# Optimization experiments

Measured on AMD Instinct MI355X. Metric: run time of the kernel, lower is better.

Reference implementation:

```python
import jax, jax.numpy as jnp
import numpy as np

NB1, NB2, B1 = 4, 4, 48
IN_F, OUT_F = 4096, 4096
BATCH = 16384


def setup_inputs() -> dict:
    key = jax.random.key(0)
    k1, k2, k3, k4 = jax.random.split(key, 4)
    i = IN_F // NB1          # 1024, per-block input width
    l = OUT_F // NB2         # 1024, per-block output width
    x = jax.random.normal(k1, (BATCH, IN_F), jnp.float32)
    # kaiming-uniform-ish scale for the factors
    w1_bfly = jax.random.normal(k2, (NB1, NB2 * B1, i), jnp.float32) * (1.0 / np.sqrt(i))
    w2_bfly = jax.random.normal(k3, (NB2, l, NB1 * B1), jnp.float32) * (1.0 / np.sqrt(NB1 * B1))
    bias = jax.random.normal(k4, (OUT_F,), jnp.float32) * 0.01
    return {"x": x, "w1_bfly": w1_bfly, "w2_bfly": w2_bfly, "bias": bias}


def reference(x, w1_bfly, w2_bfly, bias):
    # blockdiag_butterfly_multiply_einsum (Monarch-style, two block-diagonal GEMMs)
    k, q, p = w1_bfly.shape   # k = nblocks1, q = nblocks2*b1, p = in/nblocks1
    l, s, r = w2_bfly.shape   # l = nblocks2, s = out/nblocks2, r = nblocks1*b1
    b1 = q // l
    batch = x.shape[0]
    xr = x.reshape(batch, k, p)
    # stage 1: block-diagonal matmul over nblocks1
    out1 = jnp.einsum('bkp,kqp->bkq', xr, w1_bfly)               # (b, k, l*b1)
    # block transpose: (b, k, (l b1)) -> (b, l, (k b1))
    out1 = out1.reshape(batch, k, l, b1).transpose(0, 2, 1, 3).reshape(batch, l, k * b1)
    # stage 2: block-diagonal matmul over nblocks2
    out2 = jnp.einsum('blr,lsr->bls', out1, w2_bfly)             # (b, l, s)
    return out2.reshape(batch, l * s) + bias
```

## Files before the change

kernel.cpp:

```cpp
#include <hip/hip_runtime.h>
#include <cstdint>
#include <cstddef>

typedef __attribute__((ext_vector_type(8))) short short8;
typedef __attribute__((ext_vector_type(4))) float f32x4;
typedef __attribute__((ext_vector_type(4))) short short4v;

__device__ __forceinline__ unsigned short f2bf(float f) {
  unsigned u = __builtin_bit_cast(unsigned, f);
  u += 0x7fffu + ((u >> 16) & 1u);
  return (unsigned short)(u >> 16);
}

__device__ __forceinline__ void gload_lds16(const unsigned short* g, unsigned short* l) {
  __builtin_amdgcn_global_load_lds(
      (__attribute__((address_space(1))) unsigned int*)g,
      (__attribute__((address_space(3))) unsigned int*)l, 16, 0, 0);
}

__global__ __launch_bounds__(256) void cvt_k(const float* __restrict__ src,
                                             unsigned short* __restrict__ dst, int n) {
  int i = (blockIdx.x * 256 + threadIdx.x) * 4;
  if (i + 3 < n) {
    float4 v = *(const float4*)(src + i);
    short4v o;
    o.x = (short)f2bf(v.x); o.y = (short)f2bf(v.y);
    o.z = (short)f2bf(v.z); o.w = (short)f2bf(v.w);
    *(short4v*)(dst + i) = o;
  }
}

__global__ __launch_bounds__(256, 4) void stage1_k(
    const float* __restrict__ x, const unsigned short* __restrict__ w1bf,
    unsigned short* __restrict__ Y) {
  __shared__ __attribute__((aligned(16))) unsigned short sh[(64 + 192) * 64];
  unsigned short* As = sh;
  unsigned short* Bs = sh + 64 * 64;
  const int t  = threadIdx.x;
  const int r0 = blockIdx.x * 64;
  const int kb = blockIdx.y;

  const int lane = t & 63;
  const int w  = t >> 6;
  const int wm = w & 1, wn = w >> 1;
  const int lm = lane & 15;
  const int lk = lane >> 4;

  f32x4 acc[2][6];
#pragma unroll
  for (int i = 0; i < 2; ++i)
#pragma unroll
    for (int j = 0; j < 6; ++j) acc[i][j] = (f32x4)0.0f;

  const float* xbase = x + (size_t)r0 * 4096 + kb * 1024;
  const unsigned short* wb = w1bf + (size_t)kb * 192 * 1024;
  const int ldsbase = (t & ~63) << 3;

  for (int kt = 0; kt < 16; ++kt) {
    const int k0 = kt * 64;
#pragma unroll
    for (int i = 0; i < 6; ++i) {
      int c = i * 256 + t;
      int row = c >> 3, slot = c & 7;
      gload_lds16(wb + (size_t)row * 1024 + k0 + ((slot ^ (row & 7)) << 3),
                  Bs + (i * 256 << 3) + ldsbase);
    }
#pragma unroll
    for (int j = 0; j < 2; ++j) {
      int u = t + 256 * j;
      int row = u >> 3, c8 = u & 7;
      const float* p = xbase + (size_t)row * 4096 + k0 + c8 * 8;
      float4 a0 = *(const float4*)p;
      float4 a1 = *(const float4*)(p + 4);
      short8 o;
      o[0] = (short)f2bf(a0.x); o[1] = (short)f2bf(a0.y);
      o[2] = (short)f2bf(a0.z); o[3] = (short)f2bf(a0.w);
      o[4] = (short)f2bf(a1.x); o[5] = (short)f2bf(a1.y);
      o[6] = (short)f2bf(a1.z); o[7] = (short)f2bf(a1.w);
      *(short8*)&As[(row << 6) + ((c8 ^ (row & 7)) << 3)] = o;
    }
    __syncthreads();
#pragma unroll
    for (int ks = 0; ks < 2; ++ks) {
      const int sl = ks * 4 + lk;
      short8 a[2], b[6];
#pragma unroll
      for (int rt = 0; rt < 2; ++rt) {
        int r = wm * 32 + rt * 16 + lm;
        a[rt] = *(const short8*)&As[(r << 6) + ((sl ^ (r & 7)) << 3)];
      }
#pragma unroll
      for (int ct = 0; ct < 6; ++ct) {
        int r = wn * 96 + ct * 16 + lm;
        b[ct] = *(const short8*)&Bs[(r << 6) + ((sl ^ (r & 7)) << 3)];
      }
#pragma unroll
      for (int rt = 0; rt < 2; ++rt)
#pragma unroll
        for (int ct = 0; ct < 6; ++ct)
          acc[rt][ct] = __builtin_amdgcn_mfma_f32_16x16x32_bf16(a[rt], b[ct], acc[rt][ct], 0, 0, 0);
    }
    __syncthreads();
  }

#pragma unroll
  for (int rt = 0; rt < 2; ++rt) {
#pragma unroll
    for (int ct = 0; ct < 6; ++ct) {
      int q  = wn * 96 + ct * 16 + lm;
      int li = q / 48, j = q - li * 48;
      size_t base = (size_t)(r0 + wm * 32 + rt * 16 + lk * 4) * 768 + li * 192 + kb * 48 + j;
#pragma unroll
      for (int reg = 0; reg < 4; ++reg)
        Y[base + (size_t)reg * 768] = f2bf(acc[rt][ct][reg]);
    }
  }
}

__global__ __launch_bounds__(256, 4) void stage2_k(
    const unsigned short* __restrict__ Y, const unsigned short* __restrict__ w2bf,
    const float* __restrict__ bias, float* __restrict__ out) {
  __shared__ __attribute__((aligned(16))) unsigned short sh[2 * 128 * 64];
  unsigned short* As = sh;
  unsigned short* Bs = sh + 128 * 64;

  int lin  = blockIdx.x;
  int virt = ((lin & 7) << 9) + (lin >> 3);
  const int n0 = (virt & 7) * 128;
  const int r0 = ((virt >> 3) & 127) * 128;
  const int l  = virt >> 10;

  const int t = threadIdx.x;
  const int lane = t & 63;
  const int w  = t >> 6;
  const int wm = w & 1, wn = w >> 1;
  const int lm = lane & 15;
  const int lk = lane >> 4;

  f32x4 acc[4][4];
#pragma unroll
  for (int i = 0; i < 4; ++i)
#pragma unroll
    for (int j = 0; j < 4; ++j) acc[i][j] = (f32x4)0.0f;

  const unsigned short* ybase = Y + (size_t)r0 * 768 + l * 192;
  const unsigned short* wbase = w2bf + (size_t)(l * 1024 + n0) * 192;
  const int ldsbase = (t & ~63) << 3;

  for (int kt = 0; kt < 3; ++kt) {
    const int k0 = kt * 64;
#pragma unroll
    for (int i = 0; i < 4; ++i) {
      int c = i * 256 + t;
      int row = c >> 3, slot = c & 7;
      int sc = k0 + ((slot ^ (row & 7)) << 3);
      gload_lds16(ybase + (size_t)row * 768 + sc, As + (i * 256 << 3) + ldsbase);
      gload_lds16(wbase + (size_t)row * 192 + sc, Bs + (i * 256 << 3) + ldsbase);
    }
    __syncthreads();
#pragma unroll
    for (int ks = 0; ks < 2; ++ks) {
      const int sl = ks * 4 + lk;
      short8 a[4], b[4];
#pragma unroll
      for (int rt = 0; rt < 4; ++rt) {
        int r = wm * 64 + rt * 16 + lm;
        a[rt] = *(const short8*)&As[(r << 6) + ((sl ^ (r & 7)) << 3)];
      }
#pragma unroll
      for (int ct = 0; ct < 4; ++ct) {
        int r = wn * 64 + ct * 16 + lm;
        b[ct] = *(const short8*)&Bs[(r << 6) + ((sl ^ (r & 7)) << 3)];
      }
#pragma unroll
      for (int rt = 0; rt < 4; ++rt)
#pragma unroll
        for (int ct = 0; ct < 4; ++ct)
          acc[rt][ct] = __builtin_amdgcn_mfma_f32_16x16x32_bf16(a[rt], b[ct], acc[rt][ct], 0, 0, 0);
    }
    __syncthreads();
  }

  float* LF = (float*)sh + w * 1088;
  float bv[4];
#pragma unroll
  for (int ct = 0; ct < 4; ++ct)
    bv[ct] = bias[l * 1024 + n0 + wn * 64 + ct * 16 + lm];

#pragma unroll
  for (int rt = 0; rt < 4; ++rt) {
#pragma unroll
    for (int ct = 0; ct < 4; ++ct)
#pragma unroll
      for (int reg = 0; reg < 4; ++reg)
        LF[(lk * 4 + reg) * 68 + ct * 16 + lm] = acc[rt][ct][reg] + bv[ct];
#pragma unroll
    for (int it = 0; it < 4; ++it) {
      int idx = it * 64 + lane;
      int rr = idx >> 4, cc = idx & 15;
      float4 vv = *(const float4*)&LF[rr * 68 + cc * 4];
      *(float4*)&out[(size_t)(r0 + wm * 64 + rt * 16 + rr) * 4096 + l * 1024 + n0 + wn * 64 + cc * 4] = vv;
    }
  }
}

extern "C" void kernel_launch(void* const* d_in, const int* in_sizes, int n_in,
                              void* d_out, int out_size, void* d_ws, size_t ws_size,
                              hipStream_t stream) {
  const float* x    = (const float*)d_in[0];
  const float* w1   = (const float*)d_in[1];
  const float* w2   = (const float*)d_in[2];
  const float* bias = (const float*)d_in[3];
  float* out = (float*)d_out;

  unsigned short* Y    = (unsigned short*)d_ws;
  unsigned short* w1bf = (unsigned short*)((char*)d_ws + 25165824);
  unsigned short* w2bf = (unsigned short*)((char*)d_ws + 25165824 + 1572864);

  cvt_k<<<768, 256, 0, stream>>>(w1, w1bf, 786432);
  cvt_k<<<768, 256, 0, stream>>>(w2, w2bf, 786432);
  stage1_k<<<dim3(256, 4), 256, 0, stream>>>(x, w1bf, Y);
  stage2_k<<<4096, 256, 0, stream>>>(Y, w2bf, bias, out);
}
```

Measured before the change: 508.7 us.

## Fuse both butterfly GEMM stages into one kernel keeping intermediate in LDS

Merges the stage-1 and stage-2 kernels into a single kernel where each block handles 32 rows, computes all four stage-1 blocks into a swizzled LDS tile, then runs stage 2 from that LDS tile with B fragments read straight from global memory. This removes the global round-trip of the bf16 intermediate and one launch, and the two weight-conversion launches are merged into one. It also adds register prefetch of the next x tile. In exchange the grid is only 512 blocks with 2 per CU, the M tile is small, which lowers weight reuse, and output stores are scalar and uncoalesced.

```diff
diff --git a/kernel.cpp b/kernel.cpp
--- a/kernel.cpp
+++ b/kernel.cpp
@@ -18,189 +18,151 @@
       (__attribute__((address_space(3))) unsigned int*)l, 16, 0, 0);
 }
 
-__global__ __launch_bounds__(256) void cvt_k(const float* __restrict__ src,
-                                             unsigned short* __restrict__ dst, int n) {
+__global__ __launch_bounds__(256) void cvt_k(const float* __restrict__ w1,
+                                             const float* __restrict__ w2,
+                                             unsigned short* __restrict__ w1bf,
+                                             unsigned short* __restrict__ w2bf) {
+  const float* src = blockIdx.y ? w2 : w1;
+  unsigned short* dst = blockIdx.y ? w2bf : w1bf;
   int i = (blockIdx.x * 256 + threadIdx.x) * 4;
-  if (i + 3 < n) {
-    float4 v = *(const float4*)(src + i);
-    short4v o;
-    o.x = (short)f2bf(v.x); o.y = (short)f2bf(v.y);
-    o.z = (short)f2bf(v.z); o.w = (short)f2bf(v.w);
-    *(short4v*)(dst + i) = o;
-  }
+  float4 v = *(const float4*)(src + i);
+  short4v o;
+  o.x = (short)f2bf(v.x); o.y = (short)f2bf(v.y);
+  o.z = (short)f2bf(v.z); o.w = (short)f2bf(v.w);
+  *(short4v*)(dst + i) = o;
 }
 
-__global__ __launch_bounds__(256, 4) void stage1_k(
+#define YT_SH (32 * 768)
+__global__ __launch_bounds__(256, 2) void fused_k(
     const float* __restrict__ x, const unsigned short* __restrict__ w1bf,
-    unsigned short* __restrict__ Y) {
-  __shared__ __attribute__((aligned(16))) unsigned short sh[(64 + 192) * 64];
-  unsigned short* As = sh;
-  unsigned short* Bs = sh + 64 * 64;
-  const int t  = threadIdx.x;
-  const int r0 = blockIdx.x * 64;
-  const int kb = blockIdx.y;
+    const unsigned short* __restrict__ w2bf, const float* __restrict__ bias,
+    float* __restrict__ out) {
+  __shared__ __attribute__((aligned(16))) unsigned short sh[YT_SH + 2048 + 12288];
+  unsigned short* Yt = sh;
+  unsigned short* As = sh + YT_SH;
+  unsigned short* Bs = sh + YT_SH + 2048;
 
+  const int t    = threadIdx.x;
+  const int r0   = blockIdx.x * 32;
   const int lane = t & 63;
-  const int w  = t >> 6;
+  const int w    = t >> 6;
   const int wm = w & 1, wn = w >> 1;
-  const int lm = lane & 15;
-  const int lk = lane >> 4;
+  const int lm = lane & 15, lk = lane >> 4;
 
-  f32x4 acc[2][6];
-#pragma unroll
-  for (int i = 0; i < 2; ++i)
-#pragma unroll
-    for (int j = 0; j < 6; ++j) acc[i][j] = (f32x4)0.0f;
-
-  const float* xbase = x + (size_t)r0 * 4096 + kb * 1024;
-  const unsigned short* wb = w1bf + (size_t)kb * 192 * 1024;
+  const int arow = t >> 3, ac8 = t & 7;
+  const float* xrow = x + (size_t)(r0 + arow) * 4096 + ac8 * 8;
   const int ldsbase = (t & ~63) << 3;
 
-  for (int kt = 0; kt < 16; ++kt) {
-    const int k0 = kt * 64;
+  float4 px0 = *(const float4*)(xrow);
+  float4 px1 = *(const float4*)(xrow + 4);
+
+  for (int kb = 0; kb < 4; ++kb) {
+    f32x4 acc[6];
 #pragma unroll
-    for (int i = 0; i < 6; ++i) {
-      int c = i * 256 + t;
-      int row = c >> 3, slot = c & 7;
-      gload_lds16(wb + (size_t)row * 1024 + k0 + ((slot ^ (row & 7)) << 3),
-                  Bs + (i * 256 << 3) + ldsbase);
-    }
+    for (int j = 0; j < 6; ++j) acc[j] = (f32x4)0.0f;
+    const unsigned short* wb = w1bf + (size_t)kb * 192 * 1024;
+
+    for (int kt = 0; kt < 16; ++kt) {
+      const int k0 = kt * 64;
 #pragma unroll
-    for (int j = 0; j < 2; ++j) {
-      int u = t + 256 * j;
-      int row = u >> 3, c8 = u & 7;
-      const float* p = xbase + (size_t)row * 4096 + k0 + c8 * 8;
-      float4 a0 = *(const float4*)p;
-      float4 a1 = *(const float4*)(p + 4);
+      for (int i = 0; i < 6; ++i) {
+        int c = i * 256 + t;
+        int row = c >> 3, slot = c & 7;
+        gload_lds16(wb + (size_t)row * 1024 + k0 + ((slot ^ (row & 7)) << 3),
+                    Bs + (i * 256 << 3) + ldsbase);
+      }
       short8 o;
-      o[0] = (short)f2bf(a0.x); o[1] = (short)f2bf(a0.y);
-      o[2] = (short)f2bf(a0.z); o[3] = (short)f2bf(a0.w);
-      o[4] = (short)f2bf(a1.x); o[5] = (short)f2bf(a1.y);
-      o[6] = (short)f2bf(a1.z); o[7] = (short)f2bf(a1.w);
-      *(short8*)&As[(row << 6) + ((c8 ^ (row & 7)) << 3)] = o;
-    }
-    __syncthreads();
-#pragma unroll
-    for (int ks = 0; ks < 2; ++ks) {
-      const int sl = ks * 4 + lk;
-      short8 a[2], b[6];
-#pragma unroll
-      for (int rt = 0; rt < 2; ++rt) {
-        int r = wm * 32 + rt * 16 + lm;
-        a[rt] = *(const short8*)&As[(r << 6) + ((sl ^ (r & 7)) << 3)];
+      o[0] = (short)f2bf(px0.x); o[1] = (short)f2bf(px0.y);
+      o[2] = (short)f2bf(px0.z); o[3] = (short)f2bf(px0.w);
+      o[4] = (short)f2bf(px1.x); o[5] = (short)f2bf(px1.y);
+      o[6] = (short)f2bf(px1.z); o[7] = (short)f2bf(px1.w);
+      *(short8*)&As[(arow << 6) + ((ac8 ^ (arow & 7)) << 3)] = o;
+      __syncthreads();
+      int nk = kb * 16 + kt + 1;
+      if (nk < 64) {
+        const float* p = xrow + (nk >> 4) * 1024 + (nk & 15) * 64;
+        px0 = *(const float4*)p;
+        px1 = *(const float4*)(p + 4);
       }
 #pragma unroll
-      for (int ct = 0; ct < 6; ++ct) {
-        int r = wn * 96 + ct * 16 + lm;
-        b[ct] = *(const short8*)&Bs[(r << 6) + ((sl ^ (r & 7)) << 3)];
+      for (int ks = 0; ks < 2; ++ks) {
+        const int sl = ks * 4 + lk;
+        const int ra = wm * 16 + lm;
+        short8 a = *(const short8*)&As[(ra << 6) + ((sl ^ (ra & 7)) << 3)];
+#pragma unroll
+        for (int ct = 0; ct < 6; ++ct) {
+          int rb = wn * 96 + ct * 16 + lm;
+          short8 b = *(const short8*)&Bs[(rb << 6) + ((sl ^ (rb & 7)) << 3)];
+          acc[ct] = __builtin_amdgcn_mfma_f32_16x16x32_bf16(a, b, acc[ct], 0, 0, 0);
+        }
       }
-#pragma unroll
-      for (int rt = 0; rt < 2; ++rt)
-#pragma unroll
-        for (int ct = 0; ct < 6; ++ct)
-          acc[rt][ct] = __builtin_amdgcn_mfma_f32_16x16x32_bf16(a[rt], b[ct], acc[rt][ct], 0, 0, 0);
+      asm volatile("s_waitcnt lgkmcnt(0)" ::: "memory");
+      __builtin_amdgcn_s_barrier();
+      __builtin_amdgcn_sched_barrier(0);
+      asm volatile("" ::: "memory");
     }
-    __syncthreads();
-  }
-
-#pragma unroll
-  for (int rt = 0; rt < 2; ++rt) {
 #pragma unroll
     for (int ct = 0; ct < 6; ++ct) {
       int q  = wn * 96 + ct * 16 + lm;
       int li = q / 48, j = q - li * 48;
-      size_t base = (size_t)(r0 + wm * 32 + rt * 16 + lk * 4) * 768 + li * 192 + kb * 48 + j;
+      int ycol  = li * 192 + kb * 48 + j;
+      int yslot = ycol >> 3, yoff = ycol & 7;
 #pragma unroll
-      for (int reg = 0; reg < 4; ++reg)
-        Y[base + (size_t)reg * 768] = f2bf(acc[rt][ct][reg]);
+      for (int reg = 0; reg < 4; ++reg) {
+        int row = wm * 16 + lk * 4 + reg;
+        Yt[row * 768 + ((yslot ^ (row & 7)) << 3) + yoff] = f2bf(acc[ct][reg]);
+      }
     }
   }
-}
 
-__global__ __launch_bounds__(256, 4) void stage2_k(
-    const unsigned short* __restrict__ Y, const unsigned short* __restrict__ w2bf,
-    const float* __restrict__ bias, float* __restrict__ out) {
-  __shared__ __attribute__((aligned(16))) unsigned short sh[2 * 128 * 64];
-  unsigned short* As = sh;
-  unsigned short* Bs = sh + 128 * 64;
+  __syncthreads();
 
-  int lin  = blockIdx.x;
-  int virt = ((lin & 7) << 9) + (lin >> 3);
-  const int n0 = (virt & 7) * 128;
-  const int r0 = ((virt >> 3) & 127) * 128;
-  const int l  = virt >> 10;
+  const int l = w;
+  const unsigned short* w2b = w2bf + (size_t)l * 1024 * 192;
 
-  const int t = threadIdx.x;
-  const int lane = t & 63;
-  const int w  = t >> 6;
-  const int wm = w & 1, wn = w >> 1;
-  const int lm = lane & 15;
-  const int lk = lane >> 4;
+  short8 af[2][6];
+#pragma unroll
+  for (int rt = 0; rt < 2; ++rt)
+#pragma unroll
+    for (int ks = 0; ks < 6; ++ks) {
+      int row  = rt * 16 + lm;
+      int slot = l * 24 + ks * 4 + lk;
+      af[rt][ks] = *(const short8*)&Yt[row * 768 + ((slot ^ (row & 7)) << 3)];
+    }
 
-  f32x4 acc[4][4];
+  for (int nc = 0; nc < 16; ++nc) {
+    const int n0 = nc * 64;
+    f32x4 acc[2][4];
 #pragma unroll
-  for (int i = 0; i < 4; ++i)
+    for (int rt = 0; rt < 2; ++rt)
 #pragma unroll
-    for (int j = 0; j < 4; ++j) acc[i][j] = (f32x4)0.0f;
+      for (int ct = 0; ct < 4; ++ct) acc[rt][ct] = (f32x4)0.0f;
 
-  const unsigned short* ybase = Y + (size_t)r0 * 768 + l * 192;
-  const unsigned short* wbase = w2bf + (size_t)(l * 1024 + n0) * 192;
-  const int ldsbase = (t & ~63) << 3;
-
-  for (int kt = 0; kt < 3; ++kt) {
-    const int k0 = kt * 64;
 #pragma unroll
-    for (int i = 0; i < 4; ++i) {
-      int c = i * 256 + t;
-      int row = c >> 3, slot = c & 7;
-      int sc = k0 + ((slot ^ (row & 7)) << 3);
-      gload_lds16(ybase + (size_t)row * 768 + sc, As + (i * 256 << 3) + ldsbase);
-      gload_lds16(wbase + (size_t)row * 192 + sc, Bs + (i * 256 << 3) + ldsbase);
-    }
-    __syncthreads();
+    for (int ks = 0; ks < 6; ++ks) {
+      short8 b[4];
 #pragma unroll
-    for (int ks = 0; ks < 2; ++ks) {
-      const int sl = ks * 4 + lk;
-      short8 a[4], b[4];
+      for (int ct = 0; ct < 4; ++ct)
+        b[ct] = *(const short8*)(w2b + (size_t)(n0 + ct * 16 + lm) * 192 + ks * 32 + lk * 8);
 #pragma unroll
-      for (int rt = 0; rt < 4; ++rt) {
-        int r = wm * 64 + rt * 16 + lm;
-        a[rt] = *(const short8*)&As[(r << 6) + ((sl ^ (r & 7)) << 3)];
-      }
-#pragma unroll
-      for (int ct = 0; ct < 4; ++ct) {
-        int r = wn * 64 + ct * 16 + lm;
-        b[ct] = *(const short8*)&Bs[(r << 6) + ((sl ^ (r & 7)) << 3)];
-      }
-#pragma unroll
-      for (int rt = 0; rt < 4; ++rt)
+      for (int rt = 0; rt < 2; ++rt)
 #pragma unroll
         for (int ct = 0; ct < 4; ++ct)
-          acc[rt][ct] = __builtin_amdgcn_mfma_f32_16x16x32_bf16(a[rt], b[ct], acc[rt][ct], 0, 0, 0);
+          acc[rt][ct] = __builtin_amdgcn_mfma_f32_16x16x32_bf16(af[rt][ks], b[ct], acc[rt][ct], 0, 0, 0);
     }
-    __syncthreads();
-  }
 
-  float* LF = (float*)sh + w * 1088;
-  float bv[4];
-#pragma unroll
-  for (int ct = 0; ct < 4; ++ct)
-    bv[ct] = bias[l * 1024 + n0 + wn * 64 + ct * 16 + lm];
-
-#pragma unroll
-  for (int rt = 0; rt < 4; ++rt) {
+    float bv[4];
 #pragma unroll
     for (int ct = 0; ct < 4; ++ct)
+      bv[ct] = bias[l * 1024 + n0 + ct * 16 + lm];
 #pragma unroll
-      for (int reg = 0; reg < 4; ++reg)
-        LF[(lk * 4 + reg) * 68 + ct * 16 + lm] = acc[rt][ct][reg] + bv[ct];
+    for (int rt = 0; rt < 2; ++rt)
 #pragma unroll
-    for (int it = 0; it < 4; ++it) {
-      int idx = it * 64 + lane;
-      int rr = idx >> 4, cc = idx & 15;
-      float4 vv = *(const float4*)&LF[rr * 68 + cc * 4];
-      *(float4*)&out[(size_t)(r0 + wm * 64 + rt * 16 + rr) * 4096 + l * 1024 + n0 + wn * 64 + cc * 4] = vv;
-    }
+      for (int ct = 0; ct < 4; ++ct)
+#pragma unroll
+        for (int reg = 0; reg < 4; ++reg)
+          out[(size_t)(r0 + rt * 16 + lk * 4 + reg) * 4096 + l * 1024 + n0 + ct * 16 + lm] =
+              acc[rt][ct][reg] + bv[ct];
   }
 }
 
@@ -213,12 +175,9 @@
   const float* bias = (const float*)d_in[3];
   float* out = (float*)d_out;
 
-  unsigned short* Y    = (unsigned short*)d_ws;
-  unsigned short* w1bf = (unsigned short*)((char*)d_ws + 25165824);
-  unsigned short* w2bf = (unsigned short*)((char*)d_ws + 25165824 + 1572864);
+  unsigned short* w1bf = (unsigned short*)d_ws;
+  unsigned short* w2bf = (unsigned short*)((char*)d_ws + 1572864);
 
-  cvt_k<<<768, 256, 0, stream>>>(w1, w1bf, 786432);
-  cvt_k<<<768, 256, 0, stream>>>(w2, w2bf, 786432);
-  stage1_k<<<dim3(256, 4), 256, 0, stream>>>(x, w1bf, Y);
-  stage2_k<<<4096, 256, 0, stream>>>(Y, w2bf, bias, out);
+  cvt_k<<<dim3(768, 2), 256, 0, stream>>>(w1, w2, w1bf, w2bf);
+  fused_k<<<512, 256, 0, stream>>>(x, w1bf, w2bf, bias, out);
 }
```

Measured after the change: 605.5 us. 19.0% more time.
